# Kernel optimization log

Hardware: AMD Instinct MI355X
Metric: run time of the kernel (lower is better)

## Reference

```python
import jax, jax.numpy as jnp
import numpy as np

SCALES = [1.0, 0.9, 0.8, 0.7, 0.6]  # [1 - i/10 for i in range(level=5)]
RES_SCALE = 1.0


def conv2d(x, w, b, pad):
    # NCHW conv, OIHW weights, stride 1, symmetric padding
    y = jax.lax.conv_general_dilated(
        x, w, window_strides=(1, 1), padding=[(pad, pad), (pad, pad)],
        dimension_numbers=("NCHW", "OIHW", "NCHW"))
    return y + b[None, :, None, None]


def _cubic_kernel(d, a=-0.75):
    # torch-style bicubic kernel (a = -0.75)
    d = jnp.abs(d)
    w1 = ((a + 2.0) * d - (a + 3.0)) * d * d + 1.0          # |d| <= 1
    w2 = (((a * d) - 5.0 * a) * d + 8.0 * a) * d - 4.0 * a  # 1 < |d| < 2
    return jnp.where(d <= 1.0, w1, jnp.where(d < 2.0, w2, 0.0))


def _resize_axis(x, out_size, axis):
    in_size = x.shape[axis]
    scale = in_size / out_size
    src = (jnp.arange(out_size, dtype=jnp.float32) + 0.5) * scale - 0.5  # align_corners=False
    x0 = jnp.floor(src)
    t = src - x0
    x0 = x0.astype(jnp.int32)
    out = 0.0
    bshape = [1] * x.ndim
    bshape[axis] = out_size
    for off in range(-1, 3):
        idx = jnp.clip(x0 + off, 0, in_size - 1)  # border replicate
        wgt = _cubic_kernel(t - off).reshape(bshape)
        out = out + jnp.take(x, idx, axis=axis) * wgt
    return out


def bicubic(x, oh, ow):
    return _resize_axis(_resize_axis(x, oh, 2), ow, 3)


def setup_inputs() -> dict:
    key = jax.random.key(0)
    ks = jax.random.split(key, 7)
    C, Cr = 64, 32  # channel=64, reduction=2
    x = jax.random.normal(ks[0], (4, C, 48, 48), dtype=jnp.float32)
    wb = jax.random.normal(ks[1], (Cr, C, 3, 3), dtype=jnp.float32) * 0.05  # conv_match_L_base
    bb = jax.random.normal(ks[2], (Cr,), dtype=jnp.float32) * 0.05
    wm = jax.random.normal(ks[3], (Cr, C, 3, 3), dtype=jnp.float32) * 0.05  # conv_match
    bm = jax.random.normal(ks[4], (Cr,), dtype=jnp.float32) * 0.05
    wa = jax.random.normal(ks[5], (C, C, 1, 1), dtype=jnp.float32) * 0.05   # conv_assembly
    ba = jax.random.normal(ks[6], (C,), dtype=jnp.float32) * 0.05
    return {"x": x, "wb": wb, "bb": bb, "wm": wm, "bm": bm, "wa": wa, "ba": ba}


def reference(x, wb, bb, wm, bm, wa, ba):
    N, C, H, W = x.shape
    mb = conv2d(x, wb, bb, 1)                           # [N,Cr,H,W]
    Cr = mb.shape[1]
    mb = mb.reshape(N, Cr, H * W).transpose(0, 2, 1)    # [N,HW,Cr]  (queries)
    raws, keys = [], []
    for s in SCALES:
        ref = x if s == 1.0 else bicubic(x, int(H * s), int(W * s))
        raws.append(conv2d(ref, wa, ba, 0).reshape(N, C, -1))   # values [N,C,HiWi]
        keys.append(conv2d(ref, wm, bm, 1).reshape(N, Cr, -1))  # keys   [N,Cr,HiWi]
    pyr = jnp.concatenate(keys, axis=-1)                        # [N,Cr,L]
    raw = jnp.concatenate(raws, axis=-1).transpose(0, 2, 1)     # [N,L,C]
    score = jax.nn.softmax(jnp.einsum("nqc,ncl->nql", mb, pyr), axis=-1)  # [N,HW,L]
    y = jnp.einsum("nql,nlc->nqc", score, raw)                  # [N,HW,C]
    y = y.transpose(0, 2, 1).reshape(N, C, H, W)
    return y * RES_SCALE + x
```

## Files before the change

### kernel.cpp

```cpp
#include <hip/hip_runtime.h>
#include <math.h>

typedef unsigned short ushort_t;
typedef __attribute__((ext_vector_type(8))) short short8;
typedef __attribute__((ext_vector_type(4))) float float4v;

#define NB 4
#define C 64
#define CR 32
#define HW 2304
#define LTOT 7470
#define LPAD 7472
#define NSEG 12
#define SEG 640
#define LOG2E 1.44269504088896f

#define YP_F 0
#define LP_F 7077888
#define MBBF_F   8985600
#define KEYBF_F  9133056
#define RAWTBF_F 9611136
#define WPK_F    10567552
#define WPQ_F    10576768
#define WPV_F    10585984

static __device__ __forceinline__ ushort_t f2bf(float f) {
  union { float f; unsigned u; } v; v.f = f;
  unsigned r = v.u + 0x7FFF + ((v.u >> 16) & 1);
  return (ushort_t)(r >> 16);
}

__device__ __forceinline__ float cubicw(float d) {
  float ad = fabsf(d);
  float w1 = (1.25f * ad - 2.25f) * ad * ad + 1.0f;
  float w2 = ((-0.75f * ad + 3.75f) * ad - 6.0f) * ad + 3.0f;
  return ad <= 1.0f ? w1 : (ad < 2.0f ? w2 : 0.0f);
}

__global__ __launch_bounds__(256) void k_prep(const float* __restrict__ x,
    const float* __restrict__ wm, const float* __restrict__ wb,
    const float* __restrict__ wa, ushort_t* __restrict__ xt,
    ushort_t* __restrict__ wpk, ushort_t* __restrict__ wpq,
    ushort_t* __restrict__ wpv) {
  __shared__ float tile[64][49];
  int bx = blockIdx.x, t = threadIdx.x;

  if (bx < 98) {
    int item = bx * 256 + t;
    if (item < 24960) {
      int pxslot = item >> 3, c8 = item & 7;
      int n = pxslot / 780, rr = pxslot % 780;
      int Dp, PDD, pixb, r;
      if (rr < 196)      { Dp = 50; PDD = 2500; pixb = 0;     r = rr; }
      else if (rr < 372) { Dp = 45; PDD = 2025; pixb = 10000; r = rr - 196; }
      else if (rr < 528) { Dp = 40; PDD = 1600; pixb = 18100; r = rr - 372; }
      else if (rr < 664) { Dp = 35; PDD = 1225; pixb = 24500; r = rr - 528; }
      else               { Dp = 30; PDD = 900;  pixb = 29400; r = rr - 664; }
      int py, px;
      if (r < Dp)            { py = 0; px = r; }
      else if (r < 2 * Dp)   { py = Dp - 1; px = r - Dp; }
      else { int s = r - 2 * Dp; py = 1 + (s >> 1); px = (s & 1) ? Dp - 1 : 0; }
      uint4 z = {0u, 0u, 0u, 0u};
      *(uint4*)(xt + ((size_t)(pixb + n * PDD + py * Dp + px)) * 64 + c8 * 8) = z;
    }
  } else if (bx < 290) {
    int pb = bx - 98;
    int py = pb % 48, n = pb / 48;
#pragma unroll
    for (int i = 0; i < 12; i++) {
      int idx = i * 256 + t;
      int c = idx / 48, px = idx % 48;
      tile[c][px] = x[(size_t)(n * 64 + c) * HW + py * 48 + px];
    }
    __syncthreads();
#pragma unroll
    for (int i = 0; i < 12; i++) {
      int idx = i * 256 + t;
      int c = idx & 63, px = idx >> 6;
      xt[(size_t)(n * 2500 + (py + 1) * 50 + px + 1) * 64 + c] = f2bf(tile[c][px]);
    }
  } else if (bx < 5456) {
    int tid = (bx - 290) * 256 + t;
    if (tid >= 1322496) return;
    int D, Dp, PDD, rem, pixb;
    if (tid < 473344)       { D = 43; Dp = 45; PDD = 2025; rem = tid;           pixb = 10000; }
    else if (tid < 843008)  { D = 38; Dp = 40; PDD = 1600; rem = tid - 473344;  pixb = 18100; }
    else if (tid < 1121792) { D = 33; Dp = 35; PDD = 1225; rem = tid - 843008;  pixb = 24500; }
    else                    { D = 28; Dp = 30; PDD = 900;  rem = tid - 1121792; pixb = 29400; }
    int DD = D * D;
    int pix = rem % DD, nc = rem / DD;
    int py = pix / D, px = pix % D;
    float scale = 48.0f / (float)D;
    float sy = ((float)py + 0.5f) * scale - 0.5f;
    float sx = ((float)px + 0.5f) * scale - 0.5f;
    float y0f = floorf(sy), x0f = floorf(sx);
    int y0 = (int)y0f, x0 = (int)x0f;
    float ty = sy - y0f, tx = sx - x0f;
    float wy[4], wxv[4];
#pragma unroll
    for (int k = 0; k < 4; k++) {
      wy[k]  = cubicw(ty - (float)(k - 1));
      wxv[k] = cubicw(tx - (float)(k - 1));
    }
    const float* src = x + (size_t)nc * HW;
    float acc = 0.f;
#pragma unroll
    for (int dy = 0; dy < 4; ++dy) {
      int iy = min(max(y0 - 1 + dy, 0), 47);
      const float* row = src + iy * 48;
      float a = 0.f;
#pragma unroll
      for (int dx = 0; dx < 4; ++dx) {
        int ix = min(max(x0 - 1 + dx, 0), 47);
        a = fmaf(wxv[dx], row[ix], a);
      }
      acc = fmaf(wy[dy], a, acc);
    }
    int n = nc >> 6, c = nc & 63;
    xt[(size_t)(pixb + n * PDD + (py + 1) * Dp + (px + 1)) * 64 + c] = f2bf(acc);
  } else {
    int tid = (bx - 5456) * 256 + t;
    if (tid >= 5120) return;
    int lane = tid & 63, col = lane & 15, kg = lane >> 4;
    if (tid < 4608) {
      int f = (tid >> 6) % 36;
      bool isq = tid >= 2304;
      int tap = f >> 2, half = (f >> 1) & 1, crt = f & 1;
      int cr = crt * 16 + col;
      int ic0 = half * 32 + kg * 8;
      const float* w = isq ? wb : wm;
      short8 v;
#pragma unroll
      for (int j = 0; j < 8; j++) v[j] = (short)f2bf(w[cr * 576 + (ic0 + j) * 9 + tap]);
      *(short8*)((isq ? wpq : wpk) + (size_t)f * 512 + lane * 8) = v;
    } else {
      int id = tid - 4608;
      int f = id >> 6;
      int half = f >> 2, vt = f & 3;
      int c = vt * 16 + col, ic0 = half * 32 + kg * 8;
      short8 v;
#pragma unroll
      for (int j = 0; j < 8; j++) v[j] = (short)f2bf(wa[c * 64 + ic0 + j]);
      *(short8*)(wpv + (size_t)f * 512 + lane * 8) = v;
    }
  }
}

__global__ __launch_bounds__(256) void k_conv(const ushort_t* __restrict__ xt,
    const ushort_t* __restrict__ wpk, const ushort_t* __restrict__ wpq,
    const ushort_t* __restrict__ wpv, const float* __restrict__ bm,
    const float* __restrict__ bb, const float* __restrict__ ba,
    ushort_t* __restrict__ keybf, ushort_t* __restrict__ mbbf,
    ushort_t* __restrict__ rawtbf) {
  int t = threadIdx.x;
  int unit = blockIdx.x * 4 + (t >> 6);
  if (unit >= 938) return;
  int lane = t & 63, col = lane & 15, quad = lane >> 4;
  int n = blockIdx.y;
  int tile = unit >> 1, crt = unit & 1;
  int D, Dp, PDD, DD, pixb, lb, tloc;
  if (tile < 144)      { D = 48; Dp = 50; PDD = 2500; DD = 2304; pixb = 0;     lb = 0;    tloc = tile; }
  else if (tile < 260) { D = 43; Dp = 45; PDD = 2025; DD = 1849; pixb = 10000; lb = 2304; tloc = tile - 144; }
  else if (tile < 351) { D = 38; Dp = 40; PDD = 1600; DD = 1444; pixb = 18100; lb = 4153; tloc = tile - 260; }
  else if (tile < 420) { D = 33; Dp = 35; PDD = 1225; DD = 1089; pixb = 24500; lb = 5597; tloc = tile - 351; }
  else                 { D = 28; Dp = 30; PDD = 900;  DD = 784;  pixb = 29400; lb = 6686; tloc = tile - 420; }
  bool lvl0 = (tile < 144);

  int p = tloc * 16 + col;
  int pv = min(p, DD - 1);
  int py = pv / D, px = pv - py * D;
  const ushort_t* xb = xt + ((size_t)(pixb + n * PDD + (py + 1) * Dp + (px + 1))) * 64 + quad * 8;

  float4v Dk = {0.f, 0.f, 0.f, 0.f};
  float4v Dq = {0.f, 0.f, 0.f, 0.f};
  float4v Dv0 = {0.f, 0.f, 0.f, 0.f};
  float4v Dv1 = {0.f, 0.f, 0.f, 0.f};

#pragma unroll
  for (int dy = -1; dy <= 1; dy++) {
#pragma unroll
    for (int dx = -1; dx <= 1; dx++) {
      int tap = (dy + 1) * 3 + (dx + 1);
      const ushort_t* ab = xb + (dy * Dp + dx) * 64;
#pragma unroll
      for (int half = 0; half < 2; half++) {
        short8 A = *(const short8*)(ab + half * 32);
        int f = (tap * 2 + half) * 2 + crt;
        short8 Bk = *(const short8*)(wpk + (size_t)f * 512 + lane * 8);
        Dk = __builtin_amdgcn_mfma_f32_16x16x32_bf16(A, Bk, Dk, 0, 0, 0);
        if (lvl0) {
          short8 Bq = *(const short8*)(wpq + (size_t)f * 512 + lane * 8);
          Dq = __builtin_amdgcn_mfma_f32_16x16x32_bf16(A, Bq, Dq, 0, 0, 0);
        }
        if (tap == 4) {
          short8 Bv0 = *(const short8*)(wpv + (size_t)(half * 4 + crt * 2) * 512 + lane * 8);
          short8 Bv1 = *(const short8*)(wpv + (size_t)(half * 4 + crt * 2 + 1) * 512 + lane * 8);
          Dv0 = __builtin_amdgcn_mfma_f32_16x16x32_bf16(A, Bv0, Dv0, 0, 0, 0);
          Dv1 = __builtin_amdgcn_mfma_f32_16x16x32_bf16(A, Bv1, Dv1, 0, 0, 0);
        }
      }
    }
  }

  float biask = bm[crt * 16 + col];
  float biasq = bb[crt * 16 + col];
  float biasv0 = ba[crt * 32 + col];
  float biasv1 = ba[crt * 32 + 16 + col];
  int prow = tloc * 16 + quad * 4;
#pragma unroll
  for (int r = 0; r < 4; r++) {
    if (prow + r < DD) {
      int l = lb + prow + r;
      keybf[(size_t)(n * LTOT + l) * 32 + crt * 16 + col] = f2bf(Dk[r] + biask);
      if (lvl0) mbbf[(size_t)(n * HW + l) * 32 + crt * 16 + col] = f2bf((Dq[r] + biasq) * LOG2E);
      rawtbf[(size_t)(n * 64 + crt * 32 + col) * LPAD + l] = f2bf(Dv0[r] + biasv0);
      rawtbf[(size_t)(n * 64 + crt * 32 + 16 + col) * LPAD + l] = f2bf(Dv1[r] + biasv1);
    }
  }
}

__global__ __launch_bounds__(256, 4) void k_attn(const ushort_t* __restrict__ mb,
    const ushort_t* __restrict__ keyb, const ushort_t* __restrict__ rawt,
    float* __restrict__ Yp, float* __restrict__ lp) {
  __shared__ __align__(16) ushort_t VsF[2][4096];
  __shared__ __align__(16) ushort_t Pq[4][32 * 72];

  int t = threadIdx.x;
  int n = blockIdx.y, seg = blockIdx.z;
  int lane = t & 63, wv = t >> 6;
  int col = lane & 15, quad = lane >> 4;
  int qb = blockIdx.x * 128 + wv * 32;
  int l_begin = seg * SEG;
  int l_end = min(l_begin + SEG, LTOT);
  int nfull = (l_end - l_begin) >> 6;
  int rem = (l_end - l_begin) & 63;
  int nch = nfull + (rem ? 1 : 0);

  const ushort_t* keyn = keyb + (size_t)n * LTOT * CR;
  const ushort_t* rawn = rawt + (size_t)n * C * LPAD;

  short8 qA0 = *(const short8*)(mb + ((size_t)(n * HW + qb + col)) * CR + quad * 8);
  short8 qA1 = *(const short8*)(mb + ((size_t)(n * HW + qb + 16 + col)) * CR + quad * 8);

  int ct0 = (t >> 6) & 3, g0 = (t >> 4) & 3, cc0 = t & 15;
  size_t so0 = (size_t)(ct0 * 16 + cc0) * LPAD + g0 * 8;
  const ushort_t* kbase = keyn + (size_t)col * CR + quad * 8;

  float4v Y0[4], Y1[4];
#pragma unroll
  for (int ct = 0; ct < 4; ct++)
#pragma unroll
    for (int r = 0; r < 4; r++) { Y0[ct][r] = 0.f; Y1[ct][r] = 0.f; }
  float ls0 = 0.f, ls1 = 0.f;
  const float4v zero4 = {0.f, 0.f, 0.f, 0.f};
  ushort_t* Pw = Pq[wv];

  uint4 va = *(const uint4*)(rawn + so0 + l_begin);
  uint4 vb = *(const uint4*)(rawn + so0 + 32 + l_begin);
  short8 kfc[4];
#pragma unroll
  for (int tt = 0; tt < 4; tt++)
    kfc[tt] = *(const short8*)(kbase + (size_t)(l_begin + tt * 16) * CR);
  int buf = 0;

  for (int ch = 0; ch < nch; ++ch) {
    int l0 = l_begin + ch * 64;
    *(uint4*)&VsF[buf][t * 8] = va;
    *(uint4*)&VsF[buf][(t + 256) * 8] = vb;
    short8 kfn[4];
    if (ch + 1 < nch) {
      int ln = l0 + 64;
      va = *(const uint4*)(rawn + so0 + ln);
      vb = *(const uint4*)(rawn + so0 + 32 + ln);
#pragma unroll
      for (int tt = 0; tt < 4; tt++)
        kfn[tt] = *(const short8*)(kbase + (size_t)(ln + tt * 16) * CR);
    }
    __syncthreads();

    bool tail = (rem != 0) && (ch == nfull);
#pragma unroll
    for (int tt = 0; tt < 4; tt++) {
      float4v S0 = __builtin_amdgcn_mfma_f32_16x16x32_bf16(kfc[tt], qA0, zero4, 0, 0, 0);
      float4v S1 = __builtin_amdgcn_mfma_f32_16x16x32_bf16(kfc[tt], qA1, zero4, 0, 0, 0);
      int lbase = tt * 16 + quad * 4;
      float p0[4], p1[4];
#pragma unroll
      for (int r = 0; r < 4; r++) {
        bool ok = !tail || (lbase + r < rem);
        float a = __builtin_amdgcn_exp2f(S0[r]);
        float b = __builtin_amdgcn_exp2f(S1[r]);
        p0[r] = ok ? a : 0.f;
        p1[r] = ok ? b : 0.f;
        ls0 += p0[r];
        ls1 += p1[r];
      }
      union { float f; unsigned u; } c0, c1;
      uint2 w;
      c0.f = p0[0]; c1.f = p0[1];
      w.x = ((c0.u + 0x8000u) >> 16) | ((c1.u + 0x8000u) & 0xFFFF0000u);
      c0.f = p0[2]; c1.f = p0[3];
      w.y = ((c0.u + 0x8000u) >> 16) | ((c1.u + 0x8000u) & 0xFFFF0000u);
      *(uint2*)&Pw[col * 72 + lbase] = w;
      c0.f = p1[0]; c1.f = p1[1];
      w.x = ((c0.u + 0x8000u) >> 16) | ((c1.u + 0x8000u) & 0xFFFF0000u);
      c0.f = p1[2]; c1.f = p1[3];
      w.y = ((c0.u + 0x8000u) >> 16) | ((c1.u + 0x8000u) & 0xFFFF0000u);
      *(uint2*)&Pw[(16 + col) * 72 + lbase] = w;
    }

#pragma unroll
    for (int kt = 0; kt < 2; kt++) {
      short8 a0 = *(const short8*)&Pw[col * 72 + kt * 32 + quad * 8];
      short8 a1 = *(const short8*)&Pw[(16 + col) * 72 + kt * 32 + quad * 8];
#pragma unroll
      for (int ct = 0; ct < 4; ct++) {
        short8 bV = *(const short8*)&VsF[buf][(((kt << 2) | ct) * 64 + lane) * 8];
        Y0[ct] = __builtin_amdgcn_mfma_f32_16x16x32_bf16(a0, bV, Y0[ct], 0, 0, 0);
        Y1[ct] = __builtin_amdgcn_mfma_f32_16x16x32_bf16(a1, bV, Y1[ct], 0, 0, 0);
      }
    }
#pragma unroll
    for (int tt = 0; tt < 4; tt++) kfc[tt] = kfn[tt];
    buf ^= 1;
  }

  ls0 += __shfl_xor(ls0, 16); ls0 += __shfl_xor(ls0, 32);
  ls1 += __shfl_xor(ls1, 16); ls1 += __shfl_xor(ls1, 32);

  float* yo = Yp + ((size_t)(seg * NB + n) * HW + qb) * C;
#pragma unroll
  for (int ct = 0; ct < 4; ct++)
#pragma unroll
    for (int r = 0; r < 4; r++) {
      yo[(quad * 4 + r) * C + ct * 16 + col] = Y0[ct][r];
      yo[(16 + quad * 4 + r) * C + ct * 16 + col] = Y1[ct][r];
    }
  if (quad == 0) {
    int base = (seg * NB + n) * HW + qb;
    lp[base + col] = ls0;
    lp[base + 16 + col] = ls1;
  }
}

__global__ void k_combine(const float* __restrict__ x, const float* __restrict__ ws,
                          float* __restrict__ out) {
  int tid = blockIdx.x * 256 + threadIdx.x;
  int c = tid & 63;
  int t2 = tid >> 6;
  int q = t2 % HW;
  int n = t2 / HW;
  const float* Yv = ws + YP_F;
  const float* lpv = ws + LP_F;
  int i0 = n * HW + q;
  float den = 0.f, num = 0.f;
#pragma unroll
  for (int s = 0; s < NSEG; s++) {
    int idx = s * NB * HW + i0;
    den += lpv[idx];
    num += Yv[(size_t)idx * C + c];
  }
  int oi = (n * C + c) * HW + q;
  out[oi] = num / den + x[oi];
}

extern "C" void kernel_launch(void* const* d_in, const int* in_sizes, int n_in,
                              void* d_out, int out_size, void* d_ws, size_t ws_size,
                              hipStream_t stream) {
  const float* x  = (const float*)d_in[0];
  const float* wb = (const float*)d_in[1];
  const float* bb = (const float*)d_in[2];
  const float* wm = (const float*)d_in[3];
  const float* bm = (const float*)d_in[4];
  const float* wa = (const float*)d_in[5];
  const float* ba = (const float*)d_in[6];
  float* out = (float*)d_out;
  float* ws = (float*)d_ws;
  ushort_t* xt     = (ushort_t*)ws;
  ushort_t* mbbf   = (ushort_t*)(ws + MBBF_F);
  ushort_t* keybf  = (ushort_t*)(ws + KEYBF_F);
  ushort_t* rawtbf = (ushort_t*)(ws + RAWTBF_F);
  ushort_t* wpk    = (ushort_t*)(ws + WPK_F);
  ushort_t* wpq    = (ushort_t*)(ws + WPQ_F);
  ushort_t* wpv    = (ushort_t*)(ws + WPV_F);

  k_prep<<<5476, 256, 0, stream>>>(x, wm, wb, wa, xt, wpk, wpq, wpv);
  k_conv<<<dim3(235, 4), 256, 0, stream>>>(xt, wpk, wpq, wpv, bm, bb, ba,
                                           keybf, mbbf, rawtbf);
  k_attn<<<dim3(18, 4, NSEG), 256, 0, stream>>>(mbbf, keybf, rawtbf,
      ws + YP_F, ws + LP_F);
  k_combine<<<2304, 256, 0, stream>>>(x, ws, out);
}
```

Baseline: 147.4 us.

## Software-pipeline attention loop: overlap S/exp of next chunk with PV of previous

Restructures the attention chunk loop so that each iteration computes scores and exponentials for chunk ch while doing the P·V MFMAs for chunk ch-1. The probability tile is double-buffered in shared memory, with a prologue, a loop unrolled by two, and an epilogue. The goal is to let exp/convert ALU work overlap with matrix-core work and to drop one barrier per iteration. In exchange it uses more LDS (a second P buffer), which may lower occupancy, and it raises register pressure.

```diff
diff --git a/kernel.cpp b/kernel.cpp
--- a/kernel.cpp
+++ b/kernel.cpp
@@ -223,7 +223,8 @@
     const ushort_t* __restrict__ keyb, const ushort_t* __restrict__ rawt,
     float* __restrict__ Yp, float* __restrict__ lp) {
   __shared__ __align__(16) ushort_t VsF[2][4096];
-  __shared__ __align__(16) ushort_t Pq[4][32 * 72];
+  __shared__ __align__(16) ushort_t Pq0[4 * 2304];
+  __shared__ __align__(16) ushort_t Pq1[4 * 2304];
 
   int t = threadIdx.x;
   int n = blockIdx.y, seg = blockIdx.z;
@@ -253,77 +254,112 @@
     for (int r = 0; r < 4; r++) { Y0[ct][r] = 0.f; Y1[ct][r] = 0.f; }
   float ls0 = 0.f, ls1 = 0.f;
   const float4v zero4 = {0.f, 0.f, 0.f, 0.f};
-  ushort_t* Pw = Pq[wv];
+  ushort_t* Pw0 = Pq0 + wv * 2304;
+  ushort_t* Pw1 = Pq1 + wv * 2304;
 
   uint4 va = *(const uint4*)(rawn + so0 + l_begin);
   uint4 vb = *(const uint4*)(rawn + so0 + 32 + l_begin);
-  short8 kfc[4];
+  short8 kfc[4], kfn[4];
 #pragma unroll
   for (int tt = 0; tt < 4; tt++)
     kfc[tt] = *(const short8*)(kbase + (size_t)(l_begin + tt * 16) * CR);
-  int buf = 0;
-
-  for (int ch = 0; ch < nch; ++ch) {
-    int l0 = l_begin + ch * 64;
-    *(uint4*)&VsF[buf][t * 8] = va;
-    *(uint4*)&VsF[buf][(t + 256) * 8] = vb;
-    short8 kfn[4];
-    if (ch + 1 < nch) {
-      int ln = l0 + 64;
-      va = *(const uint4*)(rawn + so0 + ln);
-      vb = *(const uint4*)(rawn + so0 + 32 + ln);
-#pragma unroll
-      for (int tt = 0; tt < 4; tt++)
-        kfn[tt] = *(const short8*)(kbase + (size_t)(ln + tt * 16) * CR);
-    }
-    __syncthreads();
-
-    bool tail = (rem != 0) && (ch == nfull);
-#pragma unroll
-    for (int tt = 0; tt < 4; tt++) {
-      float4v S0 = __builtin_amdgcn_mfma_f32_16x16x32_bf16(kfc[tt], qA0, zero4, 0, 0, 0);
-      float4v S1 = __builtin_amdgcn_mfma_f32_16x16x32_bf16(kfc[tt], qA1, zero4, 0, 0, 0);
-      int lbase = tt * 16 + quad * 4;
-      float p0[4], p1[4];
-#pragma unroll
-      for (int r = 0; r < 4; r++) {
-        bool ok = !tail || (lbase + r < rem);
-        float a = __builtin_amdgcn_exp2f(S0[r]);
-        float b = __builtin_amdgcn_exp2f(S1[r]);
-        p0[r] = ok ? a : 0.f;
-        p1[r] = ok ? b : 0.f;
-        ls0 += p0[r];
-        ls1 += p1[r];
-      }
-      union { float f; unsigned u; } c0, c1;
-      uint2 w;
-      c0.f = p0[0]; c1.f = p0[1];
-      w.x = ((c0.u + 0x8000u) >> 16) | ((c1.u + 0x8000u) & 0xFFFF0000u);
-      c0.f = p0[2]; c1.f = p0[3];
-      w.y = ((c0.u + 0x8000u) >> 16) | ((c1.u + 0x8000u) & 0xFFFF0000u);
-      *(uint2*)&Pw[col * 72 + lbase] = w;
-      c0.f = p1[0]; c1.f = p1[1];
-      w.x = ((c0.u + 0x8000u) >> 16) | ((c1.u + 0x8000u) & 0xFFFF0000u);
-      c0.f = p1[2]; c1.f = p1[3];
-      w.y = ((c0.u + 0x8000u) >> 16) | ((c1.u + 0x8000u) & 0xFFFF0000u);
-      *(uint2*)&Pw[(16 + col) * 72 + lbase] = w;
-    }
-
-#pragma unroll
-    for (int kt = 0; kt < 2; kt++) {
-      short8 a0 = *(const short8*)&Pw[col * 72 + kt * 32 + quad * 8];
-      short8 a1 = *(const short8*)&Pw[(16 + col) * 72 + kt * 32 + quad * 8];
-#pragma unroll
-      for (int ct = 0; ct < 4; ct++) {
-        short8 bV = *(const short8*)&VsF[buf][(((kt << 2) | ct) * 64 + lane) * 8];
-        Y0[ct] = __builtin_amdgcn_mfma_f32_16x16x32_bf16(a0, bV, Y0[ct], 0, 0, 0);
-        Y1[ct] = __builtin_amdgcn_mfma_f32_16x16x32_bf16(a1, bV, Y1[ct], 0, 0, 0);
-      }
-    }
-#pragma unroll
-    for (int tt = 0; tt < 4; tt++) kfc[tt] = kfn[tt];
-    buf ^= 1;
-  }
+
+#define STAGE(BW) do { \
+    *(uint4*)&VsF[BW][t * 8] = va; \
+    *(uint4*)&VsF[BW][(t + 256) * 8] = vb; \
+  } while (0)
+
+#define PREFETCH(CH) do { \
+    if ((CH) + 1 < nch) { \
+      int ln_ = l_begin + ((CH) + 1) * 64; \
+      va = *(const uint4*)(rawn + so0 + ln_); \
+      vb = *(const uint4*)(rawn + so0 + 32 + ln_); \
+      _Pragma("unroll") for (int tt = 0; tt < 4; tt++) \
+        kfn[tt] = *(const short8*)(kbase + (size_t)(ln_ + tt * 16) * CR); \
+    } \
+  } while (0)
+
+#define S_PHASE(CH, PWPTR) do { \
+    bool tail_ = (rem != 0) && ((CH) == nfull); \
+    _Pragma("unroll") \
+    for (int tt = 0; tt < 4; tt++) { \
+      float4v S0 = __builtin_amdgcn_mfma_f32_16x16x32_bf16(kfc[tt], qA0, zero4, 0, 0, 0); \
+      float4v S1 = __builtin_amdgcn_mfma_f32_16x16x32_bf16(kfc[tt], qA1, zero4, 0, 0, 0); \
+      int lbase = tt * 16 + quad * 4; \
+      float p0[4], p1[4]; \
+      _Pragma("unroll") \
+      for (int r = 0; r < 4; r++) { \
+        bool ok = !tail_ || (lbase + r < rem); \
+        float ea = __builtin_amdgcn_exp2f(S0[r]); \
+        float eb = __builtin_amdgcn_exp2f(S1[r]); \
+        p0[r] = ok ? ea : 0.f; \
+        p1[r] = ok ? eb : 0.f; \
+        ls0 += p0[r]; ls1 += p1[r]; \
+      } \
+      union { float f; unsigned u; } c0_, c1_; uint2 w_; \
+      c0_.f = p0[0]; c1_.f = p0[1]; \
+      w_.x = ((c0_.u + 0x8000u) >> 16) | ((c1_.u + 0x8000u) & 0xFFFF0000u); \
+      c0_.f = p0[2]; c1_.f = p0[3]; \
+      w_.y = ((c0_.u + 0x8000u) >> 16) | ((c1_.u + 0x8000u) & 0xFFFF0000u); \
+      *(uint2*)&PWPTR[col * 72 + lbase] = w_; \
+      c0_.f = p1[0]; c1_.f = p1[1]; \
+      w_.x = ((c0_.u + 0x8000u) >> 16) | ((c1_.u + 0x8000u) & 0xFFFF0000u); \
+      c0_.f = p1[2]; c1_.f = p1[3]; \
+      w_.y = ((c0_.u + 0x8000u) >> 16) | ((c1_.u + 0x8000u) & 0xFFFF0000u); \
+      *(uint2*)&PWPTR[(16 + col) * 72 + lbase] = w_; \
+    } \
+  } while (0)
+
+#define PV_ONLY(PRPTR, BR) do { \
+    _Pragma("unroll") \
+    for (int kt = 0; kt < 2; kt++) { \
+      short8 a0_ = *(const short8*)&PRPTR[col * 72 + kt * 32 + quad * 8]; \
+      short8 a1_ = *(const short8*)&PRPTR[(16 + col) * 72 + kt * 32 + quad * 8]; \
+      _Pragma("unroll") \
+      for (int ct = 0; ct < 4; ct++) { \
+        short8 bV_ = *(const short8*)&VsF[BR][(((kt << 2) | ct) * 64 + lane) * 8]; \
+        Y0[ct] = __builtin_amdgcn_mfma_f32_16x16x32_bf16(a0_, bV_, Y0[ct], 0, 0, 0); \
+        Y1[ct] = __builtin_amdgcn_mfma_f32_16x16x32_bf16(a1_, bV_, Y1[ct], 0, 0, 0); \
+      } \
+    } \
+  } while (0)
+
+#define ROTATE() do { \
+    _Pragma("unroll") for (int tt = 0; tt < 4; tt++) kfc[tt] = kfn[tt]; \
+  } while (0)
+
+#define BODY(CH, PW, PR, BW, BR) do { \
+    STAGE(BW); \
+    PREFETCH(CH); \
+    S_PHASE(CH, PW); \
+    PV_ONLY(PR, BR); \
+    ROTATE(); \
+    __syncthreads(); \
+  } while (0)
+
+  STAGE(0);
+  PREFETCH(0);
+  S_PHASE(0, Pw0);
+  ROTATE();
+  __syncthreads();
+
+  int ch = 1;
+  for (; ch + 1 < nch; ch += 2) {
+    BODY(ch, Pw1, Pw0, 1, 0);
+    BODY(ch + 1, Pw0, Pw1, 0, 1);
+  }
+  if (ch < nch) {
+    BODY(ch, Pw1, Pw0, 1, 0);
+  }
+  if ((nch - 1) & 1) PV_ONLY(Pw1, 1);
+  else               PV_ONLY(Pw0, 0);
+
+#undef STAGE
+#undef PREFETCH
+#undef S_PHASE
+#undef PV_ONLY
+#undef ROTATE
+#undef BODY
 
   ls0 += __shfl_xor(ls0, 16); ls0 += __shfl_xor(ls0, 32);
   ls1 += __shfl_xor(ls1, 16); ls1 += __shfl_xor(ls1, 32);
```

Result: slower. 153.4 us (+4.0%).

## Halve attention block size to 128 threads and drop key register prefetch

Applied to the files above, without the earlier changes.

The attention kernel now runs 2 waves per block covering 64 queries instead of 4 waves covering 128, which doubles the grid. Each thread loads 4 V vectors per chunk into LDS instead of 2. The key fragments are no longer prefetched into registers one chunk ahead; they are loaded right before each score MFMA. The aim is more blocks for better CU coverage and fewer registers, at the cost of twice as many V loads per query and exposed key load latency.

```diff
diff --git a/kernel.cpp b/kernel.cpp
--- a/kernel.cpp
+++ b/kernel.cpp
@@ -219,17 +219,17 @@
   }
 }
 
-__global__ __launch_bounds__(256, 4) void k_attn(const ushort_t* __restrict__ mb,
+__global__ __launch_bounds__(128) void k_attn(const ushort_t* __restrict__ mb,
     const ushort_t* __restrict__ keyb, const ushort_t* __restrict__ rawt,
     float* __restrict__ Yp, float* __restrict__ lp) {
   __shared__ __align__(16) ushort_t VsF[2][4096];
-  __shared__ __align__(16) ushort_t Pq[4][32 * 72];
+  __shared__ __align__(16) ushort_t Pq[2][32 * 72];
 
   int t = threadIdx.x;
   int n = blockIdx.y, seg = blockIdx.z;
   int lane = t & 63, wv = t >> 6;
   int col = lane & 15, quad = lane >> 4;
-  int qb = blockIdx.x * 128 + wv * 32;
+  int qb = blockIdx.x * 64 + wv * 32;
   int l_begin = seg * SEG;
   int l_end = min(l_begin + SEG, LTOT);
   int nfull = (l_end - l_begin) >> 6;
@@ -242,8 +242,13 @@
   short8 qA0 = *(const short8*)(mb + ((size_t)(n * HW + qb + col)) * CR + quad * 8);
   short8 qA1 = *(const short8*)(mb + ((size_t)(n * HW + qb + 16 + col)) * CR + quad * 8);
 
-  int ct0 = (t >> 6) & 3, g0 = (t >> 4) & 3, cc0 = t & 15;
-  size_t so0 = (size_t)(ct0 * 16 + cc0) * LPAD + g0 * 8;
+  size_t so[4];
+#pragma unroll
+  for (int i = 0; i < 4; i++) {
+    int v = t + (i << 7);
+    int kt = v >> 8, ct = (v >> 6) & 3, g = (v >> 4) & 3, cc = v & 15;
+    so[i] = (size_t)(ct * 16 + cc) * LPAD + kt * 32 + g * 8;
+  }
   const ushort_t* kbase = keyn + (size_t)col * CR + quad * 8;
 
   float4v Y0[4], Y1[4];
@@ -255,34 +260,29 @@
   const float4v zero4 = {0.f, 0.f, 0.f, 0.f};
   ushort_t* Pw = Pq[wv];
 
-  uint4 va = *(const uint4*)(rawn + so0 + l_begin);
-  uint4 vb = *(const uint4*)(rawn + so0 + 32 + l_begin);
-  short8 kfc[4];
-#pragma unroll
-  for (int tt = 0; tt < 4; tt++)
-    kfc[tt] = *(const short8*)(kbase + (size_t)(l_begin + tt * 16) * CR);
+  uint4 vr[4];
+#pragma unroll
+  for (int i = 0; i < 4; i++) vr[i] = *(const uint4*)(rawn + so[i] + l_begin);
   int buf = 0;
 
   for (int ch = 0; ch < nch; ++ch) {
     int l0 = l_begin + ch * 64;
-    *(uint4*)&VsF[buf][t * 8] = va;
-    *(uint4*)&VsF[buf][(t + 256) * 8] = vb;
-    short8 kfn[4];
+#pragma unroll
+    for (int i = 0; i < 4; i++)
+      *(uint4*)&VsF[buf][(t + (i << 7)) * 8] = vr[i];
     if (ch + 1 < nch) {
       int ln = l0 + 64;
-      va = *(const uint4*)(rawn + so0 + ln);
-      vb = *(const uint4*)(rawn + so0 + 32 + ln);
-#pragma unroll
-      for (int tt = 0; tt < 4; tt++)
-        kfn[tt] = *(const short8*)(kbase + (size_t)(ln + tt * 16) * CR);
+#pragma unroll
+      for (int i = 0; i < 4; i++) vr[i] = *(const uint4*)(rawn + so[i] + ln);
     }
     __syncthreads();
 
     bool tail = (rem != 0) && (ch == nfull);
 #pragma unroll
     for (int tt = 0; tt < 4; tt++) {
-      float4v S0 = __builtin_amdgcn_mfma_f32_16x16x32_bf16(kfc[tt], qA0, zero4, 0, 0, 0);
-      float4v S1 = __builtin_amdgcn_mfma_f32_16x16x32_bf16(kfc[tt], qA1, zero4, 0, 0, 0);
+      short8 kf = *(const short8*)(kbase + (size_t)(l0 + tt * 16) * CR);
+      float4v S0 = __builtin_amdgcn_mfma_f32_16x16x32_bf16(kf, qA0, zero4, 0, 0, 0);
+      float4v S1 = __builtin_amdgcn_mfma_f32_16x16x32_bf16(kf, qA1, zero4, 0, 0, 0);
       int lbase = tt * 16 + quad * 4;
       float p0[4], p1[4];
 #pragma unroll
@@ -320,8 +320,6 @@
         Y1[ct] = __builtin_amdgcn_mfma_f32_16x16x32_bf16(a1, bV, Y1[ct], 0, 0, 0);
       }
     }
-#pragma unroll
-    for (int tt = 0; tt < 4; tt++) kfc[tt] = kfn[tt];
     buf ^= 1;
   }
 
@@ -387,7 +385,7 @@
   k_prep<<<5476, 256, 0, stream>>>(x, wm, wb, wa, xt, wpk, wpq, wpv);
   k_conv<<<dim3(235, 4), 256, 0, stream>>>(xt, wpk, wpq, wpv, bm, bb, ba,
                                            keybf, mbbf, rawtbf);
-  k_attn<<<dim3(18, 4, NSEG), 256, 0, stream>>>(mbbf, keybf, rawtbf,
+  k_attn<<<dim3(36, 4, NSEG), 128, 0, stream>>>(mbbf, keybf, rawtbf,
       ws + YP_F, ws + LP_F);
   k_combine<<<2304, 256, 0, stream>>>(x, ws, out);
 }
```

Result: slower. 179.4 us (+21.7%).
